# Kernel optimization log

Measured on AMD Instinct MI355X. Metric: run time of the kernel, lower is better.

The kernel has to match this reference:

```python
import jax, jax.numpy as jnp
import numpy as np

SEQ = 16384
HID = 1280
HEADS = 16
HEAD_DIM = HID // HEADS  # 80
NUM_WIN = 16
WIN = SEQ // NUM_WIN  # 1024


def rotate_half(x):
    x1, x2 = jnp.split(x, 2, axis=-1)
    return jnp.concatenate([-x2, x1], axis=-1)


def setup_inputs() -> dict:
    key = jax.random.key(0)
    ks = jax.random.split(key, 8)
    pos = jnp.arange(SEQ, dtype=jnp.float32)[:, None]
    inv_freq = 1.0 / (10000.0 ** (jnp.arange(0, HEAD_DIM, 2, dtype=jnp.float32) / HEAD_DIM))
    ang = pos * inv_freq[None, :]
    ang = jnp.concatenate([ang, ang], axis=-1)  # [SEQ, HEAD_DIM]
    return {
        "hidden_states": jax.random.normal(ks[0], (SEQ, HID), dtype=jnp.float32),
        "cos": jnp.cos(ang),
        "sin": jnp.sin(ang),
        "qkv_kernel": jax.random.normal(ks[1], (HID, 3 * HID), dtype=jnp.float32) * 0.02,
        "qkv_bias": jnp.zeros((3 * HID,), dtype=jnp.float32),
        "proj_kernel": jax.random.normal(ks[2], (HID, HID), dtype=jnp.float32) * 0.02,
        "proj_bias": jnp.zeros((HID,), dtype=jnp.float32),
        "cu_seqlens": jnp.arange(NUM_WIN + 1, dtype=jnp.int32) * WIN,
    }


def reference(hidden_states, cos, sin, qkv_kernel, qkv_bias, proj_kernel, proj_bias, cu_seqlens):
    seq_len = hidden_states.shape[0]
    scale = HEAD_DIM ** (-0.5)
    qkv = hidden_states @ qkv_kernel + qkv_bias
    q, k, v = jnp.split(qkv, 3, axis=-1)
    q = q.reshape(seq_len, HEADS, HEAD_DIM)
    k = k.reshape(seq_len, HEADS, HEAD_DIM)
    v = v.reshape(seq_len, HEADS, HEAD_DIM)
    c = cos[:, None, :HEAD_DIM]
    s = sin[:, None, :HEAD_DIM]
    q = q * c + rotate_half(q) * s
    k = k * c + rotate_half(k) * s
    num_win = cu_seqlens.shape[0] - 1
    win = seq_len // num_win
    qw = q.reshape(num_win, win, HEADS, HEAD_DIM).astype(jnp.float32)
    kw = k.reshape(num_win, win, HEADS, HEAD_DIM).astype(jnp.float32)
    vw = v.reshape(num_win, win, HEADS, HEAD_DIM).astype(jnp.float32)
    scores = jnp.einsum('wqhd,wkhd->whqk', qw, kw) * scale
    weights = jax.nn.softmax(scores, axis=-1)
    out = jnp.einsum('whqk,wkhd->wqhd', weights, vw)
    out = out.reshape(seq_len, HID)
    return out @ proj_kernel + proj_bias
```

## Files before the change

### kernel.cpp

```cpp
#include <hip/hip_runtime.h>
#include <stdint.h>

#define SEQ 16384
#define HIDN 1280
#define NHEADS 16
#define HD 80
#define HDP 96
#define NWIN 16
#define WINSZ 1024

typedef unsigned short u16;
typedef unsigned int u32;
typedef __bf16 bf16x8 __attribute__((ext_vector_type(8)));
typedef float f32x4 __attribute__((ext_vector_type(4)));

#define AS1 __attribute__((address_space(1)))
#define AS3 __attribute__((address_space(3)))

__device__ __forceinline__ u16 f2b(float f) {
  __bf16 h = (__bf16)f;
  return __builtin_bit_cast(u16, h);
}
__device__ __forceinline__ u32 f2b2(float lo, float hi) {
  __bf16 l = (__bf16)lo, h = (__bf16)hi;
  return (u32)__builtin_bit_cast(u16, l) | ((u32)__builtin_bit_cast(u16, h) << 16);
}
__device__ __forceinline__ float b2f(u16 u) { return __uint_as_float(((u32)u) << 16); }

__device__ __forceinline__ float fexp2(float x) {
#if __has_builtin(__builtin_amdgcn_exp2f)
  return __builtin_amdgcn_exp2f(x);
#else
  return exp2f(x);
#endif
}

__device__ __forceinline__ void load_lds16(const void* g, void* l) {
  __builtin_amdgcn_global_load_lds((AS1 void*)g, (AS3 void*)l, 16, 0, 0);
}

__global__ void k_cvt(const float* __restrict__ in, u16* __restrict__ out) {
  size_t i = ((size_t)blockIdx.x * 256 + threadIdx.x) * 4;
  float4 v = *(const float4*)(in + i);
  uint2 o;
  o.x = f2b2(v.x, v.y);
  o.y = f2b2(v.z, v.w);
  *(uint2*)(out + i) = o;
}

__global__ void k_trans(const float* __restrict__ in, u16* __restrict__ out, int R, int C) {
  __shared__ float tile[64][65];
  int c0 = blockIdx.x * 64, r0 = blockIdx.y * 64;
  int tc = threadIdx.x & 63, tr4 = threadIdx.x >> 6;
#pragma unroll
  for (int i = 0; i < 16; i++) {
    int r = tr4 + i * 4;
    tile[r][tc] = in[(size_t)(r0 + r) * C + c0 + tc];
  }
  __syncthreads();
#pragma unroll
  for (int i = 0; i < 16; i++) {
    int r = tr4 + i * 4;
    out[(size_t)(c0 + r) * R + r0 + tc] = f2b(tile[tc][r]);
  }
}


#define GBAR() asm volatile("s_barrier" ::: "memory")

template <int MODE>
__launch_bounds__(512, 2)
__global__ void k_gemm8(const u16* __restrict__ A, const u16* __restrict__ B,
                        const float* __restrict__ bias, float* __restrict__ outf,
                        u16* __restrict__ Qb, u16* __restrict__ Kb, u16* __restrict__ Vt,
                        int N, int ncol) {
  extern __shared__ char lds[];
  const int K = 1280;
  const int NT = 40;
  const int tid = threadIdx.x;
  const int wv = tid >> 6, lane = tid & 63;
  const int lr = lane & 15, lq = lane >> 4;
  const int wm = wv >> 2, wn = wv & 3;
  const int id = blockIdx.x;
  const int xs = id & 7, rest = id >> 3;
  const int cb = rest % ncol, rs = rest / ncol;
  const int row0 = (rs * 8 + xs) * 256, col0 = cb * 256;

  const u16* gA[2];
  const u16* gB[2];
  int Pst[2];
#pragma unroll
  for (int ld = 0; ld < 2; ld++) {
    int P = wv * 2048 + ld * 1024 + lane * 16;
    int j = P >> 7;
    int Wl = (P & 127) ^ ((j & 7) << 4);
    int r = 2 * j + (Wl >> 6);
    int c = (Wl & 63) >> 1;
    gA[ld] = A + (size_t)(row0 + r) * K + c;
    gB[ld] = B + (size_t)(col0 + r) * K + c;
    Pst[ld] = P;
  }

  int offA[2][4], offB[4];
#pragma unroll
  for (int ch = 0; ch < 2; ch++)
#pragma unroll
    for (int a = 0; a < 4; a++) {
      int r = wm * 128 + ch * 64 + a * 16 + lr;
      int j = r >> 1;
      int Wl = ((r & 1) << 6) | (lq << 4);
      offA[ch][a] = j * 128 + (Wl ^ ((j & 7) << 4));
    }
#pragma unroll
  for (int ni = 0; ni < 4; ni++) {
    int r = wn * 64 + ni * 16 + lr;
    int j = r >> 1;
    int Wl = ((r & 1) << 6) | (lq << 4);
    offB[ni] = 16384 + j * 128 + (Wl ^ ((j & 7) << 4));
  }

  f32x4 acc[8][4];
#pragma unroll
  for (int i = 0; i < 8; i++)
#pragma unroll
    for (int j = 0; j < 4; j++) acc[i][j] = (f32x4){0.f, 0.f, 0.f, 0.f};

#define STAGE(mat_, kt_)                                             \
  do {                                                               \
    char* lb_ = lds + (((kt_) & 3) << 15) + ((mat_) << 14);          \
    const u16* g0_ = (mat_) ? gB[0] : gA[0];                         \
    const u16* g1_ = (mat_) ? gB[1] : gA[1];                         \
    int ko_ = (kt_) * 32;                                            \
    load_lds16(g0_ + ko_, lb_ + Pst[0]);                             \
    load_lds16(g1_ + ko_, lb_ + Pst[1]);                             \
  } while (0)

#define MFMA16(dst_, af_, bf_)                                               \
  do {                                                                       \
    __builtin_amdgcn_s_setprio(1);                                           \
    _Pragma("unroll") for (int a_ = 0; a_ < 4; a_++)                         \
        _Pragma("unroll") for (int n_ = 0; n_ < 4; n_++)                     \
            acc[dst_ + a_][n_] = __builtin_amdgcn_mfma_f32_16x16x32_bf16(    \
                af_[a_], bf_[n_], acc[dst_ + a_][n_], 0, 0, 0);              \
    __builtin_amdgcn_s_setprio(0);                                           \
  } while (0)

  STAGE(0, 0);
  STAGE(1, 0);
  STAGE(0, 1);
  STAGE(1, 1);
  STAGE(0, 2);
  STAGE(1, 2);
  asm volatile("s_waitcnt vmcnt(8)" ::: "memory");
  GBAR();

#pragma unroll 4
  for (int t = 0; t < NT; t++) {
    const int bb = (t & 3) << 15;
    bf16x8 bfr[4], af0[4], af1[4];

#pragma unroll
    for (int ni = 0; ni < 4; ni++) bfr[ni] = *(const bf16x8*)(lds + bb + offB[ni]);
#pragma unroll
    for (int a = 0; a < 4; a++) af0[a] = *(const bf16x8*)(lds + bb + offA[0][a]);
    if (t + 3 < NT) STAGE(0, t + 3);
    MFMA16(0, af0, bfr);

#pragma unroll
    for (int a = 0; a < 4; a++) af1[a] = *(const bf16x8*)(lds + bb + offA[1][a]);
    if (t + 3 < NT) STAGE(1, t + 3);
    MFMA16(4, af1, bfr);

    if (t + 3 < NT)
      asm volatile("s_waitcnt vmcnt(8)" ::: "memory");
    else if (t == NT - 3)
      asm volatile("s_waitcnt vmcnt(4)" ::: "memory");
    else if (t == NT - 2)
      asm volatile("s_waitcnt vmcnt(0)" ::: "memory");
    GBAR();
  }
#undef STAGE
#undef MFMA16

#pragma unroll
  for (int ni = 0; ni < 4; ni++) {
    int col = col0 + wn * 64 + ni * 16 + lr;
    float bs = bias[col];
    if (MODE == 0) {
#pragma unroll
      for (int mi = 0; mi < 8; mi++)
#pragma unroll
        for (int r = 0; r < 4; r++) {
          int row = row0 + wm * 128 + mi * 16 + lq * 4 + r;
          outf[(size_t)row * N + col] = acc[mi][ni][r] + bs;
        }
    } else {
      int seg = col / HIDN;
      int cl = col - seg * HIDN;
      int h = cl / HD, d = cl - h * HD;
      if (seg == 2) {
#pragma unroll
        for (int mi = 0; mi < 8; mi++) {
          int row = row0 + wm * 128 + mi * 16 + lq * 4;
          uint2 o;
          o.x = f2b2(acc[mi][ni][0] + bs, acc[mi][ni][1] + bs);
          o.y = f2b2(acc[mi][ni][2] + bs, acc[mi][ni][3] + bs);
          *(uint2*)(Vt + ((size_t)h * HD + d) * SEQ + row) = o;
        }
      } else {
        u16* Dst = (seg == 0) ? Qb : Kb;
#pragma unroll
        for (int mi = 0; mi < 8; mi++)
#pragma unroll
          for (int r = 0; r < 4; r++) {
            int row = row0 + wm * 128 + mi * 16 + lq * 4 + r;
            Dst[((size_t)h * SEQ + row) * HDP + d] = f2b(acc[mi][ni][r] + bs);
          }
      }
    }
  }
}

__global__ void k_rope2(u16* __restrict__ Q, u16* __restrict__ K,
                        const float* __restrict__ cs, const float* __restrict__ sn) {
  int idx = blockIdx.x * 256 + threadIdx.x;
  const int TOT = NHEADS * SEQ * 10;
  u16* X = Q;
  if (idx >= TOT) { X = K; idx -= TOT; }
  int h = idx / (SEQ * 10);
  int rem = idx - h * (SEQ * 10);
  int s = rem / 10;
  int t = rem - s * 10;
  int d = t * 4;
  size_t base = ((size_t)h * SEQ + s) * HDP;
  float4 cv = *(const float4*)(cs + s * HD + d);
  float4 sv = *(const float4*)(sn + s * HD + d);
  uint2 a = *(const uint2*)(X + base + d);
  uint2 b = *(const uint2*)(X + base + d + 40);
  float x1[4], x2[4];
  x1[0] = b2f(a.x & 0xffffu); x1[1] = b2f(a.x >> 16);
  x1[2] = b2f(a.y & 0xffffu); x1[3] = b2f(a.y >> 16);
  x2[0] = b2f(b.x & 0xffffu); x2[1] = b2f(b.x >> 16);
  x2[2] = b2f(b.y & 0xffffu); x2[3] = b2f(b.y >> 16);
  uint2 o1, o2;
  o1.x = f2b2(x1[0] * cv.x - x2[0] * sv.x, x1[1] * cv.y - x2[1] * sv.y);
  o1.y = f2b2(x1[2] * cv.z - x2[2] * sv.z, x1[3] * cv.w - x2[3] * sv.w);
  o2.x = f2b2(x2[0] * cv.x + x1[0] * sv.x, x2[1] * cv.y + x1[1] * sv.y);
  o2.y = f2b2(x2[2] * cv.z + x1[2] * sv.z, x2[3] * cv.w + x1[3] * sv.w);
  *(uint2*)(X + base + d) = o1;
  *(uint2*)(X + base + d + 40) = o2;
  if (t < 4) {
    uint2 z; z.x = 0; z.y = 0;
    *(uint2*)(X + base + 80 + t * 4) = z;
  }
}

__launch_bounds__(256, 2)
__global__ void k_attn(const u16* __restrict__ Qb, const u16* __restrict__ Kb,
                       const u16* __restrict__ Vt, u16* __restrict__ Ob) {
  __shared__ char lds[24576 + 20480 + 4 * 4352];
  char* ldsK = lds;
  char* ldsV = lds + 24576;
  char* ldsP = lds + 45056;

  const int tid = threadIdx.x;
  const int wv = tid >> 6, lane = tid & 63;
  const int lr = lane & 15, lq = lane >> 4;

  const int b = blockIdx.x;
  const int qblk = b & 7, h = (b >> 3) & 15, w = b >> 7;
  const int q0 = w * WINSZ + qblk * 128 + wv * 32;
  const int kwin = w * WINSZ;

  bf16x8 qf[2][3];
#pragma unroll
  for (int qt = 0; qt < 2; qt++)
#pragma unroll
    for (int ds = 0; ds < 3; ds++)
      qf[qt][ds] = *(const bf16x8*)(Qb + ((size_t)h * SEQ + q0 + qt * 16 + lr) * HDP + ds * 32 + lq * 8);

  f32x4 acc[2][5];
#pragma unroll
  for (int i = 0; i < 2; i++)
#pragma unroll
    for (int j = 0; j < 5; j++) acc[i][j] = (f32x4){0.f, 0.f, 0.f, 0.f};
  float mo[2] = {-1e30f, -1e30f};
  float lsum[2] = {0.f, 0.f};
  const float kscale = 0.11180339887498949f * 1.4426950408889634f;

  for (int kt = 0; kt < 8; kt++) {
    int k0 = kwin + kt * 128;
#pragma unroll
    for (int li = 0; li < 11; li++) {
      int g = li * 4 + wv;
      const u16* gp;
      char* lp;
      if (g < 24) {
        int kt16 = g / 3, ds = g - kt16 * 3;
        gp = Kb + ((size_t)h * SEQ + k0 + kt16 * 16 + lr) * HDP + ds * 32 + lq * 8;
        lp = ldsK + g * 1024;
      } else {
        int g2 = g - 24;
        int dt = g2 >> 2, ks = g2 & 3;
        gp = Vt + ((size_t)h * HD + dt * 16 + lr) * SEQ + k0 + ks * 32 + lq * 8;
        lp = ldsV + g2 * 1024;
      }
      load_lds16(gp, lp);
    }
    __syncthreads();

    f32x4 sx[2][8];
#pragma unroll
    for (int i = 0; i < 2; i++)
#pragma unroll
      for (int j = 0; j < 8; j++) sx[i][j] = (f32x4){0.f, 0.f, 0.f, 0.f};
    __builtin_amdgcn_s_setprio(1);
#pragma unroll
    for (int kt16 = 0; kt16 < 8; kt16++) {
      bf16x8 kf0 = *(const bf16x8*)(ldsK + (kt16 * 3 + 0) * 1024 + lane * 16);
      bf16x8 kf1 = *(const bf16x8*)(ldsK + (kt16 * 3 + 1) * 1024 + lane * 16);
      bf16x8 kf2 = *(const bf16x8*)(ldsK + (kt16 * 3 + 2) * 1024 + lane * 16);
#pragma unroll
      for (int qt = 0; qt < 2; qt++) {
        sx[qt][kt16] = __builtin_amdgcn_mfma_f32_16x16x32_bf16(kf0, qf[qt][0], sx[qt][kt16], 0, 0, 0);
        sx[qt][kt16] = __builtin_amdgcn_mfma_f32_16x16x32_bf16(kf1, qf[qt][1], sx[qt][kt16], 0, 0, 0);
        sx[qt][kt16] = __builtin_amdgcn_mfma_f32_16x16x32_bf16(kf2, qf[qt][2], sx[qt][kt16], 0, 0, 0);
      }
    }
    __builtin_amdgcn_s_setprio(0);

    bf16x8 pf[2][4];
#pragma unroll
    for (int qt = 0; qt < 2; qt++) {
      float mx = -1e30f;
#pragma unroll
      for (int t = 0; t < 8; t++)
#pragma unroll
        for (int r = 0; r < 4; r++) mx = fmaxf(mx, sx[qt][t][r]);
      mx = fmaxf(mx, __shfl_xor(mx, 16));
      mx = fmaxf(mx, __shfl_xor(mx, 32));
      float mxs = mx * kscale;
      if (!__all(mxs <= mo[qt] + 8.f)) {
        float mnew = fmaxf(mo[qt], mxs);
        float alpha = fexp2(mo[qt] - mnew);
        mo[qt] = mnew;
        lsum[qt] *= alpha;
#pragma unroll
        for (int dt = 0; dt < 5; dt++) acc[qt][dt] *= alpha;
      }
      float ls = 0.f;
#pragma unroll
      for (int t = 0; t < 8; t++)
#pragma unroll
        for (int r = 0; r < 4; r++) {
          float p = fexp2(fmaf(sx[qt][t][r], kscale, -mo[qt]));
          sx[qt][t][r] = p;
          ls += p;
        }
      ls += __shfl_xor(ls, 16);
      ls += __shfl_xor(ls, 32);
      lsum[qt] += ls;
      char* pw = ldsP + wv * 4352;
#pragma unroll
      for (int t = 0; t < 8; t++) {
        uint2 o;
        o.x = f2b2(sx[qt][t][0], sx[qt][t][1]);
        o.y = f2b2(sx[qt][t][2], sx[qt][t][3]);
        *(uint2*)(pw + lr * 272 + t * 32 + lq * 8) = o;
      }
#pragma unroll
      for (int ks = 0; ks < 4; ks++)
        pf[qt][ks] = *(const bf16x8*)(pw + lr * 272 + ks * 64 + lq * 16);
    }

    __builtin_amdgcn_s_setprio(1);
#pragma unroll
    for (int dt = 0; dt < 5; dt++)
#pragma unroll
      for (int ks = 0; ks < 4; ks++) {
        bf16x8 vf = *(const bf16x8*)(ldsV + (dt * 4 + ks) * 1024 + lane * 16);
#pragma unroll
        for (int qt = 0; qt < 2; qt++)
          acc[qt][dt] = __builtin_amdgcn_mfma_f32_16x16x32_bf16(vf, pf[qt][ks], acc[qt][dt], 0, 0, 0);
      }
    __builtin_amdgcn_s_setprio(0);
    __syncthreads();
  }

#pragma unroll
  for (int qt = 0; qt < 2; qt++) {
    float rl = 1.f / lsum[qt];
    int s = q0 + qt * 16 + lr;
#pragma unroll
    for (int dt = 0; dt < 5; dt++) {
      uint2 o;
      o.x = f2b2(acc[qt][dt][0] * rl, acc[qt][dt][1] * rl);
      o.y = f2b2(acc[qt][dt][2] * rl, acc[qt][dt][3] * rl);
      size_t ob = (size_t)s * HIDN + h * HD + dt * 16 + lq * 4;
      *(uint2*)(Ob + ob) = o;
    }
  }
}

extern "C" void kernel_launch(void* const* d_in, const int* in_sizes, int n_in,
                              void* d_out, int out_size, void* d_ws, size_t ws_size,
                              hipStream_t stream) {
  (void)in_sizes; (void)n_in; (void)out_size; (void)ws_size;
  const float* hidden = (const float*)d_in[0];
  const float* cosb   = (const float*)d_in[1];
  const float* sinb   = (const float*)d_in[2];
  const float* qkvk   = (const float*)d_in[3];
  const float* qkvb   = (const float*)d_in[4];
  const float* projk  = (const float*)d_in[5];
  const float* projb  = (const float*)d_in[6];

  char* ws = (char*)d_ws;
  u16* Abf = (u16*)(ws + 0);
  u16* Wt  = (u16*)(ws + 41943040);
  u16* Pt  = (u16*)(ws + 51773440);
  u16* Qb  = (u16*)(ws + 55050240);
  u16* Kb  = (u16*)(ws + 105381888);
  u16* Vtb = (u16*)(ws + 155713536);

  static int attr_done = 0;
  if (!attr_done) {
    (void)hipFuncSetAttribute((const void*)&k_gemm8<1>,
                              hipFuncAttributeMaxDynamicSharedMemorySize, 131072);
    (void)hipFuncSetAttribute((const void*)&k_gemm8<0>,
                              hipFuncAttributeMaxDynamicSharedMemorySize, 131072);
    (void)hipGetLastError();
    attr_done = 1;
  }

  k_cvt<<<20480, 256, 0, stream>>>(hidden, Abf);
  k_trans<<<dim3(60, 20), 256, 0, stream>>>(qkvk, Wt, 1280, 3840);
  k_trans<<<dim3(20, 20), 256, 0, stream>>>(projk, Pt, 1280, 1280);
  k_gemm8<1><<<960, 512, 131072, stream>>>(Abf, Wt, qkvb, nullptr, Qb, Kb, Vtb, 3840, 15);
  k_rope2<<<20480, 256, 0, stream>>>(Qb, Kb, cosb, sinb);
  k_attn<<<2048, 256, 0, stream>>>(Qb, Kb, Vtb, Abf);
  k_gemm8<0><<<320, 512, 131072, stream>>>(Abf, Pt, projb, (float*)d_out,
                                           nullptr, nullptr, nullptr, 1280, 5);
}
```

Baseline: 598.6 us.

## Load GEMM B operand directly from global into registers, halving LDS use

The GEMM kernel no longer stages the weight (B) tile through LDS. Each wave now loads its B fragments straight from global memory into registers with global_load_dwordx4 every k-step, and only A is staged in LDS, which halves dynamic shared memory to 64KB. The kernel is templated on the number of N fragments per wave: the projection GEMM uses a narrower 128-column tile with twice as many blocks to fill more CUs. The cost is duplicated global/L2 traffic for B across the waves that share columns, and a B-load latency that is exposed each iteration because fragments are not prefetched ahead.

```diff
diff --git a/kernel.cpp b/kernel.cpp
--- a/kernel.cpp
+++ b/kernel.cpp
@@ -13,6 +13,7 @@
 typedef unsigned int u32;
 typedef __bf16 bf16x8 __attribute__((ext_vector_type(8)));
 typedef float f32x4 __attribute__((ext_vector_type(4)));
+typedef u32 u32x4 __attribute__((ext_vector_type(4)));
 
 #define AS1 __attribute__((address_space(1)))
 #define AS3 __attribute__((address_space(3)))
@@ -68,7 +69,7 @@
 
 #define GBAR() asm volatile("s_barrier" ::: "memory")
 
-template <int MODE>
+template <int MODE, int NF>
 __launch_bounds__(512, 2)
 __global__ void k_gemm8(const u16* __restrict__ A, const u16* __restrict__ B,
                         const float* __restrict__ bias, float* __restrict__ outf,
@@ -84,10 +85,9 @@
   const int id = blockIdx.x;
   const int xs = id & 7, rest = id >> 3;
   const int cb = rest % ncol, rs = rest / ncol;
-  const int row0 = (rs * 8 + xs) * 256, col0 = cb * 256;
+  const int row0 = (rs * 8 + xs) * 256, col0 = cb * (NF * 64);
 
   const u16* gA[2];
-  const u16* gB[2];
   int Pst[2];
 #pragma unroll
   for (int ld = 0; ld < 2; ld++) {
@@ -97,11 +97,10 @@
     int r = 2 * j + (Wl >> 6);
     int c = (Wl & 63) >> 1;
     gA[ld] = A + (size_t)(row0 + r) * K + c;
-    gB[ld] = B + (size_t)(col0 + r) * K + c;
     Pst[ld] = P;
   }
 
-  int offA[2][4], offB[4];
+  int offA[2][4];
 #pragma unroll
   for (int ch = 0; ch < 2; ch++)
 #pragma unroll
@@ -111,80 +110,79 @@
       int Wl = ((r & 1) << 6) | (lq << 4);
       offA[ch][a] = j * 128 + (Wl ^ ((j & 7) << 4));
     }
-#pragma unroll
-  for (int ni = 0; ni < 4; ni++) {
-    int r = wn * 64 + ni * 16 + lr;
-    int j = r >> 1;
-    int Wl = ((r & 1) << 6) | (lq << 4);
-    offB[ni] = 16384 + j * 128 + (Wl ^ ((j & 7) << 4));
-  }
-
-  f32x4 acc[8][4];
+
+  const u16* gBp[NF];
+#pragma unroll
+  for (int ni = 0; ni < NF; ni++)
+    gBp[ni] = B + (size_t)(col0 + wn * (NF * 16) + ni * 16 + lr) * K + lq * 8;
+
+  f32x4 acc[8][NF];
 #pragma unroll
   for (int i = 0; i < 8; i++)
 #pragma unroll
-    for (int j = 0; j < 4; j++) acc[i][j] = (f32x4){0.f, 0.f, 0.f, 0.f};
-
-#define STAGE(mat_, kt_)                                             \
+    for (int j = 0; j < NF; j++) acc[i][j] = (f32x4){0.f, 0.f, 0.f, 0.f};
+
+#define STAGEA(kt_)                                                  \
   do {                                                               \
-    char* lb_ = lds + (((kt_) & 3) << 15) + ((mat_) << 14);          \
-    const u16* g0_ = (mat_) ? gB[0] : gA[0];                         \
-    const u16* g1_ = (mat_) ? gB[1] : gA[1];                         \
+    char* lb_ = lds + (((kt_) & 3) << 14);                           \
     int ko_ = (kt_) * 32;                                            \
-    load_lds16(g0_ + ko_, lb_ + Pst[0]);                             \
-    load_lds16(g1_ + ko_, lb_ + Pst[1]);                             \
+    load_lds16(gA[0] + ko_, lb_ + Pst[0]);                           \
+    load_lds16(gA[1] + ko_, lb_ + Pst[1]);                           \
   } while (0)
 
-#define MFMA16(dst_, af_, bf_)                                               \
+#define MFMA16(dst_, af_)                                                    \
   do {                                                                       \
     __builtin_amdgcn_s_setprio(1);                                           \
     _Pragma("unroll") for (int a_ = 0; a_ < 4; a_++)                         \
-        _Pragma("unroll") for (int n_ = 0; n_ < 4; n_++)                     \
+        _Pragma("unroll") for (int n_ = 0; n_ < NF; n_++)                    \
             acc[dst_ + a_][n_] = __builtin_amdgcn_mfma_f32_16x16x32_bf16(    \
-                af_[a_], bf_[n_], acc[dst_ + a_][n_], 0, 0, 0);              \
+                af_[a_], bfr[n_], acc[dst_ + a_][n_], 0, 0, 0);              \
     __builtin_amdgcn_s_setprio(0);                                           \
   } while (0)
 
-  STAGE(0, 0);
-  STAGE(1, 0);
-  STAGE(0, 1);
-  STAGE(1, 1);
-  STAGE(0, 2);
-  STAGE(1, 2);
-  asm volatile("s_waitcnt vmcnt(8)" ::: "memory");
+  STAGEA(0);
+  STAGEA(1);
+  STAGEA(2);
+  asm volatile("s_waitcnt vmcnt(4)" ::: "memory");
   GBAR();
 
 #pragma unroll 4
   for (int t = 0; t < NT; t++) {
-    const int bb = (t & 3) << 15;
-    bf16x8 bfr[4], af0[4], af1[4];
-
-#pragma unroll
-    for (int ni = 0; ni < 4; ni++) bfr[ni] = *(const bf16x8*)(lds + bb + offB[ni]);
+    const int bb = (t & 3) << 14;
+    bf16x8 bfr[NF], af0[4], af1[4];
+
+#pragma unroll
+    for (int ni = 0; ni < NF; ni++) {
+      u32x4 tmp;
+      asm volatile("global_load_dwordx4 %0, %1, off"
+                   : "=v"(tmp)
+                   : "v"(gBp[ni])
+                   : "memory");
+      bfr[ni] = __builtin_bit_cast(bf16x8, tmp);
+      gBp[ni] += 32;
+    }
+    if (t + 3 < NT) {
+      STAGEA(t + 3);
+      asm volatile("s_waitcnt vmcnt(2)" ::: "memory");
+    } else {
+      asm volatile("s_waitcnt vmcnt(0)" ::: "memory");
+    }
+    __builtin_amdgcn_sched_barrier(0);
+
 #pragma unroll
     for (int a = 0; a < 4; a++) af0[a] = *(const bf16x8*)(lds + bb + offA[0][a]);
-    if (t + 3 < NT) STAGE(0, t + 3);
-    MFMA16(0, af0, bfr);
-
+    MFMA16(0, af0);
 #pragma unroll
     for (int a = 0; a < 4; a++) af1[a] = *(const bf16x8*)(lds + bb + offA[1][a]);
-    if (t + 3 < NT) STAGE(1, t + 3);
-    MFMA16(4, af1, bfr);
-
-    if (t + 3 < NT)
-      asm volatile("s_waitcnt vmcnt(8)" ::: "memory");
-    else if (t == NT - 3)
-      asm volatile("s_waitcnt vmcnt(4)" ::: "memory");
-    else if (t == NT - 2)
-      asm volatile("s_waitcnt vmcnt(0)" ::: "memory");
+    MFMA16(4, af1);
     GBAR();
   }
-#undef STAGE
+#undef STAGEA
 #undef MFMA16
 
 #pragma unroll
-  for (int ni = 0; ni < 4; ni++) {
-    int col = col0 + wn * 64 + ni * 16 + lr;
+  for (int ni = 0; ni < NF; ni++) {
+    int col = col0 + wn * (NF * 16) + ni * 16 + lr;
     float bs = bias[col];
     if (MODE == 0) {
 #pragma unroll
@@ -424,10 +422,10 @@
 
   static int attr_done = 0;
   if (!attr_done) {
-    (void)hipFuncSetAttribute((const void*)&k_gemm8<1>,
-                              hipFuncAttributeMaxDynamicSharedMemorySize, 131072);
-    (void)hipFuncSetAttribute((const void*)&k_gemm8<0>,
-                              hipFuncAttributeMaxDynamicSharedMemorySize, 131072);
+    (void)hipFuncSetAttribute((const void*)&k_gemm8<1, 4>,
+                              hipFuncAttributeMaxDynamicSharedMemorySize, 65536);
+    (void)hipFuncSetAttribute((const void*)&k_gemm8<0, 2>,
+                              hipFuncAttributeMaxDynamicSharedMemorySize, 65536);
     (void)hipGetLastError();
     attr_done = 1;
   }
@@ -435,9 +433,9 @@
   k_cvt<<<20480, 256, 0, stream>>>(hidden, Abf);
   k_trans<<<dim3(60, 20), 256, 0, stream>>>(qkvk, Wt, 1280, 3840);
   k_trans<<<dim3(20, 20), 256, 0, stream>>>(projk, Pt, 1280, 1280);
-  k_gemm8<1><<<960, 512, 131072, stream>>>(Abf, Wt, qkvb, nullptr, Qb, Kb, Vtb, 3840, 15);
+  k_gemm8<1, 4><<<960, 512, 65536, stream>>>(Abf, Wt, qkvb, nullptr, Qb, Kb, Vtb, 3840, 15);
   k_rope2<<<20480, 256, 0, stream>>>(Qb, Kb, cosb, sinb);
   k_attn<<<2048, 256, 0, stream>>>(Qb, Kb, Vtb, Abf);
-  k_gemm8<0><<<320, 512, 131072, stream>>>(Abf, Pt, projb, (float*)d_out,
-                                           nullptr, nullptr, nullptr, 1280, 5);
-}
+  k_gemm8<0, 2><<<640, 512, 65536, stream>>>(Abf, Pt, projb, (float*)d_out,
+                                             nullptr, nullptr, nullptr, 1280, 10);
+}
```

After: 742.5 us. 24.0% more time.
